# Kernel tuning notes

Hardware: AMD Instinct MI355X
Metric: run time of the kernel (lower is better)

Reference implementation:

```python
import jax, jax.numpy as jnp
import numpy as np

B, C, D, H, W = 1, 128, 8, 32, 32
HEADS = 4
DH = C // HEADS
SCALE = DH ** -0.5


def conv1x1(x, Wt, b):
    # 1x1x1 Conv3d == pointwise channel mix: Wt [out,in], x [B,Cin,D,H,W]
    return jnp.einsum('oc,bcdhw->bodhw', Wt, x) + b[None, :, None, None, None]


def setup_inputs() -> dict:
    key = jax.random.key(0)
    ks = jax.random.split(key, 16)
    p = lambda k, shape: jax.random.normal(k, shape, dtype=jnp.float32) * 0.02
    return {
        'feat1': jax.random.normal(ks[0], (B, C, D, H, W), dtype=jnp.float32),
        'feat2': jax.random.normal(ks[1], (B, C, D, H, W), dtype=jnp.float32),
        'Wq': p(ks[2], (C, C)), 'bq': jnp.zeros((C,), jnp.float32),
        'Wk': p(ks[3], (C, C)), 'bk': jnp.zeros((C,), jnp.float32),
        'Wv': p(ks[4], (C, C)), 'bv': jnp.zeros((C,), jnp.float32),
        'Wo': p(ks[5], (C, C)), 'bo': jnp.zeros((C,), jnp.float32),
        'Wg1': p(ks[6], (C, 2 * C)), 'bg1': jnp.zeros((C,), jnp.float32),
        'Wg2': p(ks[7], (C, C)), 'bg2': jnp.zeros((C,), jnp.float32),
    }


def reference(feat1, feat2, Wq, bq, Wk, bk, Wv, bv, Wo, bo, Wg1, bg1, Wg2, bg2):
    N = D * H * W
    q = conv1x1(feat1, Wq, bq).reshape(B, HEADS, DH, N)
    k = conv1x1(feat2, Wk, bk).reshape(B, HEADS, DH, N)
    v = conv1x1(feat2, Wv, bv).reshape(B, HEADS, DH, N)
    # attn[b,h,n,m] = softmax_m( q[:, :, :, n] . k[:, :, :, m] * scale )
    attn = jax.nn.softmax(jnp.einsum('bhcn,bhcm->bhnm', q, k) * SCALE, axis=-1)
    # out[b,h,c,n] = sum_m attn[b,h,n,m] * v[b,h,c,m]
    out = jnp.einsum('bhnm,bhcm->bhcn', attn, v).reshape(B, C, D, H, W)
    attn_out = conv1x1(out, Wo, bo)
    gated_input = jnp.concatenate([attn_out, feat1], axis=1)  # [B,2C,D,H,W]
    gate = jax.nn.sigmoid(conv1x1(jax.nn.relu(conv1x1(gated_input, Wg1, bg1)), Wg2, bg2))
    return gate * feat1 + (1.0 - gate) * attn_out
```

## Files before the change

### kernel.cpp

```cpp
#include <hip/hip_runtime.h>
#include <hip/hip_bf16.h>


typedef __attribute__((ext_vector_type(4))) float f32x4;
typedef __attribute__((ext_vector_type(4))) unsigned u32x4;
typedef __attribute__((ext_vector_type(8))) short s16x8;
typedef __attribute__((ext_vector_type(4))) short s16x4;

#define MFMA_BF16(A,B,C) __builtin_amdgcn_mfma_f32_16x16x32_bf16((A),(B),(C),0,0,0)

static __device__ __forceinline__ float fexp2(float x){
  float r; asm("v_exp_f32 %0, %1" : "=v"(r) : "v"(x)); return r;
}
static __device__ __forceinline__ float frcp(float x){
  float r; asm("v_rcp_f32 %0, %1" : "=v"(r) : "v"(x)); return r;
}
static __device__ __forceinline__ unsigned cvtpk(float lo, float hi){
  unsigned r; asm("v_cvt_pk_bf16_f32 %0, %1, %2" : "=v"(r) : "v"(lo), "v"(hi)); return r;
}
static __device__ __forceinline__ float bf2f(short s){
  return __bfloat162float(__builtin_bit_cast(__hip_bfloat16, s));
}

__device__ __forceinline__ void gll16(const void* g, void* l){
  __builtin_amdgcn_global_load_lds(
      (const __attribute__((address_space(1))) void*)g,
      (__attribute__((address_space(3))) void*)l, 16, 0, 0);
}

__global__ __launch_bounds__(256) void wprep(
    const float* __restrict__ Wq, const float* __restrict__ Wk,
    const float* __restrict__ Wv, const float* __restrict__ Wo,
    const float* __restrict__ Wg1, const float* __restrict__ Wg2,
    __hip_bfloat16* __restrict__ out)
{
  int i = blockIdx.x*256 + threadIdx.x;
  const float SCQ = 0.17677669529663689f * 1.44269504088896340f;
  float v;
  if      (i < 16384) v = Wq[i]*SCQ;
  else if (i < 32768) v = Wk[i-16384];
  else if (i < 49152) v = Wv[i-32768];
  else if (i < 65536) v = Wo[i-49152];
  else if (i < 98304) v = Wg1[i-65536];
  else                v = Wg2[i-98304];
  out[i] = __float2bfloat16(v);
}

__global__ __launch_bounds__(256) void transpose2(
    const float* __restrict__ f1, const float* __restrict__ f2,
    __hip_bfloat16* __restrict__ F1T, __hip_bfloat16* __restrict__ F2T)
{
  const float* in = blockIdx.y ? f2 : f1;
  __hip_bfloat16* out = blockIdx.y ? F2T : F1T;
  __shared__ __hip_bfloat16 tile[64][128];
  int tid = threadIdx.x;
  int n0 = blockIdx.x*64;
  int cq = tid>>4;
  int nq = (tid&15)*4;
  #pragma unroll
  for (int r=0;r<8;r++){
    int c = r*16 + cq;
    f32x4 val = *(const f32x4*)&in[c*8192 + n0 + nq];
    #pragma unroll
    for (int i=0;i<4;i++){
      int n = nq + i;
      tile[n][c ^ ((n&7)<<4)] = __float2bfloat16(val[i]);
    }
  }
  __syncthreads();
  int row = tid>>2;
  int cb  = (tid&3)*32;
  #pragma unroll
  for (int k=0;k<4;k++){
    int c0 = cb + 8*k;
    s16x8 v = *(const s16x8*)&tile[row][c0 ^ ((row&7)<<4)];
    *(s16x8*)&out[(n0+row)*128 + c0] = v;
  }
}

__global__ __launch_bounds__(256) void qkv(
    const __hip_bfloat16* __restrict__ F1T, const __hip_bfloat16* __restrict__ F2T,
    const __hip_bfloat16* __restrict__ Wall,
    const float* __restrict__ bq, const float* __restrict__ bk,
    const float* __restrict__ bv,
    __hip_bfloat16* __restrict__ QT, __hip_bfloat16* __restrict__ KT,
    __hip_bfloat16* __restrict__ Vp)
{
  const float SCQ = 0.17677669529663689f * 1.44269504088896340f;
  int y = blockIdx.y;
  const __hip_bfloat16* A  = (y==0) ? F1T : F2T;
  const __hip_bfloat16* Bw = Wall + y*16384;
  const float* bias = (y==0) ? bq : (y==1) ? bk : bv;
  float bscale = (y==0) ? SCQ : 1.f;

  int tid = threadIdx.x;
  int w = tid>>6, lane = tid&63, g = lane>>4, ln = lane&15;
  int n0 = blockIdx.x*16, o0 = w*32;
  f32x4 acc0 = {0.f,0.f,0.f,0.f}, acc1 = {0.f,0.f,0.f,0.f};
  #pragma unroll
  for (int ck=0; ck<4; ck++){
    s16x8 af  = *(const s16x8*)&A[(n0+ln)*128 + ck*32 + 8*g];
    s16x8 bf0 = *(const s16x8*)&Bw[(o0+ln)*128 + ck*32 + 8*g];
    s16x8 bf1 = *(const s16x8*)&Bw[(o0+16+ln)*128 + ck*32 + 8*g];
    if (y == 2){
      acc0 = MFMA_BF16(bf0, af, acc0);
      acc1 = MFMA_BF16(bf1, af, acc1);
    } else {
      acc0 = MFMA_BF16(af, bf0, acc0);
      acc1 = MFMA_BF16(af, bf1, acc1);
    }
  }
  if (y == 2){
    #pragma unroll
    for (int to=0; to<2; to++){
      f32x4 a = to ? acc1 : acc0;
      #pragma unroll
      for (int r=0;r<4;r++){
        int o = o0 + 16*to + 4*g + r;
        int n = n0 + ln;
        int m63 = n & 63, blk = n >> 6;
        int Gx = (((m63>>5)<<2) | ((m63>>2)&3)) ^ (o & 7);
        int col = blk*64 + Gx*8 + ((m63>>4)&1)*4 + (m63&3);
        Vp[(size_t)o*8192 + col] = __float2bfloat16(a[r] + bias[o]);
      }
    }
  } else {
    __hip_bfloat16* outb = (y==0) ? QT : KT;
    float b0 = bias[o0+ln]*bscale, b1 = bias[o0+16+ln]*bscale;
    #pragma unroll
    for (int to=0; to<2; to++){
      f32x4 a = to ? acc1 : acc0;
      float bb = to ? b1 : b0;
      int o = o0 + 16*to + ln;
      #pragma unroll
      for (int r=0;r<4;r++){
        int n = n0 + 4*g + r;
        outb[n*128 + o] = __float2bfloat16(a[r] + bb);
      }
    }
  }
}

__global__ __launch_bounds__(256, 2) void attn13(
    const __hip_bfloat16* __restrict__ QT, const __hip_bfloat16* __restrict__ KT,
    const __hip_bfloat16* __restrict__ Vp, __hip_bfloat16* __restrict__ OT)
{
  __shared__ short stage[2][8192];

  const int tid = threadIdx.x;
  const int w = tid>>6, lane = tid&63, g = lane>>4, ln = lane&15;
  const int h = blockIdx.y;
  const int nbase = blockIdx.x*64;

  const __hip_bfloat16* Kh = KT + h*32;
  const __hip_bfloat16* Vh = Vp + (size_t)(h*32)*8192;

  s16x8 qf[4];
  #pragma unroll
  for (int j=0;j<4;j++)
    qf[j] = *(const s16x8*)&QT[(size_t)(nbase+16*j+ln)*128 + h*32 + 8*g];

  const __hip_bfloat16* gp[4];
  int ldoff[4];
  #pragma unroll
  for (int u=0; u<4; u++){
    int row = u*16 + (lane>>2);
    int gk  = (lane&3) ^ ((lane>>3)&3);
    gp[u] = &Kh[(size_t)(w*2048 + row)*128 + 8*gk];
    ldoff[u] = w*2048 + u*512;
  }
  short* sb = &stage[0][0];

  #define ISSUE(OFF) { \
    _Pragma("unroll") \
    for (int u=0;u<4;u++){ gll16(gp[u], sb + (OFF) + ldoff[u]); gp[u] += 64*128; } }

  const int kloff = ln*32 + ((g ^ ((ln>>1)&3))<<3);
  int voff[2];
  voff[0] = 8*((g  ) ^ (ln&7));
  voff[1] = 8*((g+4) ^ (ln&7));

  const short* vb[2][2];
  #pragma unroll
  for (int kk=0;kk<2;kk++)
    #pragma unroll
    for (int ct=0;ct<2;ct++)
      vb[kk][ct] = (const short*)Vh + (size_t)(16*ct+ln)*8192 + w*2048 + voff[kk];

  const u32x4 onesw = {0x3F803F80u,0x3F803F80u,0x3F803F80u,0x3F803F80u};
  const s16x8 onesf = __builtin_bit_cast(s16x8, onesw);

  f32x4 acc[2][4];
  #pragma unroll
  for (int ct=0;ct<2;ct++)
    #pragma unroll
    for (int j=0;j<4;j++) acc[ct][j] = (f32x4){0.f,0.f,0.f,0.f};
  f32x4 accS[4];
  #pragma unroll
  for (int j=0;j<4;j++) accS[j] = (f32x4){0.f,0.f,0.f,0.f};

  #define CONSUME(CUR, T) { \
    const short* Kl = sb + (CUR) + w*2048; \
    s16x8 kf0 = *(const s16x8*)&Kl[         kloff]; \
    s16x8 kf1 = *(const s16x8*)&Kl[ 512  +  kloff]; \
    s16x8 kf2 = *(const s16x8*)&Kl[1024  +  kloff]; \
    s16x8 kf3 = *(const s16x8*)&Kl[1536  +  kloff]; \
    const int mo = (T)*64; \
    s16x8 vf00 = *(const s16x8*)(vb[0][0] + mo); \
    s16x8 vf01 = *(const s16x8*)(vb[0][1] + mo); \
    s16x8 vf10 = *(const s16x8*)(vb[1][0] + mo); \
    s16x8 vf11 = *(const s16x8*)(vb[1][1] + mo); \
    const f32x4 z = {0.f,0.f,0.f,0.f}; \
    __builtin_amdgcn_s_setprio(1); \
    f32x4 s00 = MFMA_BF16(kf0, qf[0], z), s01 = MFMA_BF16(kf0, qf[1], z); \
    f32x4 s02 = MFMA_BF16(kf0, qf[2], z), s03 = MFMA_BF16(kf0, qf[3], z); \
    f32x4 s10 = MFMA_BF16(kf1, qf[0], z), s11 = MFMA_BF16(kf1, qf[1], z); \
    f32x4 s12 = MFMA_BF16(kf1, qf[2], z), s13 = MFMA_BF16(kf1, qf[3], z); \
    __builtin_amdgcn_s_setprio(0); \
    s16x8 pb0[4]; \
    _Pragma("unroll") \
    for (int j=0;j<4;j++){ \
      f32x4 sa = (j==0)?s00:(j==1)?s01:(j==2)?s02:s03; \
      f32x4 sc = (j==0)?s10:(j==1)?s11:(j==2)?s12:s13; \
      float e0=fexp2(sa[0]), e1=fexp2(sa[1]), e2=fexp2(sa[2]), e3=fexp2(sa[3]); \
      float f0=fexp2(sc[0]), f1=fexp2(sc[1]), f2=fexp2(sc[2]), f3=fexp2(sc[3]); \
      u32x4 pw; \
      pw[0]=cvtpk(e0,e1); pw[1]=cvtpk(e2,e3); pw[2]=cvtpk(f0,f1); pw[3]=cvtpk(f2,f3); \
      pb0[j] = __builtin_bit_cast(s16x8, pw); \
    } \
    __builtin_amdgcn_s_setprio(1); \
    f32x4 s20 = MFMA_BF16(kf2, qf[0], z), s21 = MFMA_BF16(kf2, qf[1], z); \
    f32x4 s22 = MFMA_BF16(kf2, qf[2], z), s23 = MFMA_BF16(kf2, qf[3], z); \
    f32x4 s30 = MFMA_BF16(kf3, qf[0], z), s31 = MFMA_BF16(kf3, qf[1], z); \
    f32x4 s32 = MFMA_BF16(kf3, qf[2], z), s33 = MFMA_BF16(kf3, qf[3], z); \
    __builtin_amdgcn_s_setprio(0); \
    s16x8 pb1[4]; \
    _Pragma("unroll") \
    for (int j=0;j<4;j++){ \
      f32x4 sa = (j==0)?s20:(j==1)?s21:(j==2)?s22:s23; \
      f32x4 sc = (j==0)?s30:(j==1)?s31:(j==2)?s32:s33; \
      float e0=fexp2(sa[0]), e1=fexp2(sa[1]), e2=fexp2(sa[2]), e3=fexp2(sa[3]); \
      float f0=fexp2(sc[0]), f1=fexp2(sc[1]), f2=fexp2(sc[2]), f3=fexp2(sc[3]); \
      u32x4 pw; \
      pw[0]=cvtpk(e0,e1); pw[1]=cvtpk(e2,e3); pw[2]=cvtpk(f0,f1); pw[3]=cvtpk(f2,f3); \
      pb1[j] = __builtin_bit_cast(s16x8, pw); \
    } \
    __builtin_amdgcn_s_setprio(1); \
    _Pragma("unroll") \
    for (int j=0;j<4;j++){ \
      acc[0][j] = MFMA_BF16(vf00, pb0[j], acc[0][j]); \
      acc[1][j] = MFMA_BF16(vf01, pb0[j], acc[1][j]); \
      acc[0][j] = MFMA_BF16(vf10, pb1[j], acc[0][j]); \
      acc[1][j] = MFMA_BF16(vf11, pb1[j], acc[1][j]); \
      accS[j]   = MFMA_BF16(onesf, pb0[j], accS[j]); \
      accS[j]   = MFMA_BF16(onesf, pb1[j], accS[j]); \
    } \
    __builtin_amdgcn_s_setprio(0); \
  }

  ISSUE(0);
  int cur = 0;
  for (int t=0; t<31; ++t){
    ISSUE(8192 - cur);
    asm volatile("s_waitcnt vmcnt(4)" ::: "memory");
    CONSUME(cur, t);
    cur = 8192 - cur;
  }
  asm volatile("s_waitcnt vmcnt(0)" ::: "memory");
  CONSUME(cur, 31);
  #undef CONSUME
  #undef ISSUE

  __syncthreads();
  float* scr = (float*)sb;
  if (w != 0){
    int base = ((w-1)*64 + lane)*36;
    #pragma unroll
    for (int ct=0; ct<2; ct++)
      #pragma unroll
      for (int j=0;j<4;j++)
        *(f32x4*)&scr[base + (ct*4+j)*4] = acc[ct][j];
    #pragma unroll
    for (int j=0;j<4;j++) scr[base+32+j] = accS[j][0];
  }
  __syncthreads();
  if (w == 0){
    float inv[4];
    #pragma unroll
    for (int j=0;j<4;j++){
      float ps = accS[j][0];
      #pragma unroll
      for (int q=0; q<3; q++) ps += scr[(q*64+lane)*36 + 32 + j];
      inv[j] = frcp(ps);
    }
    #pragma unroll
    for (int ct=0; ct<2; ct++){
      #pragma unroll
      for (int j=0;j<4;j++){
        f32x4 o = acc[ct][j];
        #pragma unroll
        for (int q=0; q<3; q++)
          o += *(const f32x4*)&scr[(q*64+lane)*36 + (ct*4+j)*4];
        unsigned lo = cvtpk(o[0]*inv[j], o[1]*inv[j]);
        unsigned hi = cvtpk(o[2]*inv[j], o[3]*inv[j]);
        unsigned long long pk = ((unsigned long long)hi<<32) | lo;
        *(unsigned long long*)&OT[(size_t)(nbase+16*j+ln)*128 + h*32 + 16*ct + 4*g] = pk;
      }
    }
  }
}

__global__ __launch_bounds__(256) void tail3(
    const __hip_bfloat16* __restrict__ OT, const __hip_bfloat16* __restrict__ F1T,
    const __hip_bfloat16* __restrict__ WOb, const __hip_bfloat16* __restrict__ WG1b,
    const __hip_bfloat16* __restrict__ WG2b,
    const float* __restrict__ bo, const float* __restrict__ bg1,
    const float* __restrict__ bg2,
    const float* __restrict__ feat1, float* __restrict__ out)
{
  __shared__ __hip_bfloat16 aot[16][128];
  __shared__ __hip_bfloat16 g1[16][128];
  int tid = threadIdx.x;
  int w = tid>>6, lane = tid&63, g = lane>>4, ln = lane&15;
  int n0 = blockIdx.x*16, o0 = w*32;

  {
    f32x4 a0 = {0,0,0,0}, a1 = {0,0,0,0};
    #pragma unroll
    for (int ck=0; ck<4; ck++){
      s16x8 af  = *(const s16x8*)&OT[(n0+ln)*128 + ck*32 + 8*g];
      s16x8 bf0 = *(const s16x8*)&WOb[(o0+ln)*128 + ck*32 + 8*g];
      s16x8 bf1 = *(const s16x8*)&WOb[(o0+16+ln)*128 + ck*32 + 8*g];
      a0 = MFMA_BF16(af, bf0, a0);
      a1 = MFMA_BF16(af, bf1, a1);
    }
    float b0 = bo[o0+ln], b1 = bo[o0+16+ln];
    #pragma unroll
    for (int to=0; to<2; to++){
      f32x4 a = to ? a1 : a0;
      float bb = to ? b1 : b0;
      int o = o0 + 16*to + ln;
      #pragma unroll
      for (int r=0;r<4;r++)
        aot[4*g + r][o] = __float2bfloat16(a[r] + bb);
    }
  }
  __syncthreads();

  {
    f32x4 a0 = {0,0,0,0}, a1 = {0,0,0,0};
    #pragma unroll
    for (int ck=0; ck<8; ck++){
      s16x8 af;
      if (ck < 4) af = *(const s16x8*)&aot[ln][ck*32 + 8*g];
      else        af = *(const s16x8*)&F1T[(n0+ln)*128 + (ck-4)*32 + 8*g];
      s16x8 bf0 = *(const s16x8*)&WG1b[(o0+ln)*256 + ck*32 + 8*g];
      s16x8 bf1 = *(const s16x8*)&WG1b[(o0+16+ln)*256 + ck*32 + 8*g];
      a0 = MFMA_BF16(af, bf0, a0);
      a1 = MFMA_BF16(af, bf1, a1);
    }
    float b0 = bg1[o0+ln], b1 = bg1[o0+16+ln];
    #pragma unroll
    for (int to=0; to<2; to++){
      f32x4 a = to ? a1 : a0;
      float bb = to ? b1 : b0;
      int o = o0 + 16*to + ln;
      #pragma unroll
      for (int r=0;r<4;r++)
        g1[4*g + r][o] = __float2bfloat16(fmaxf(a[r] + bb, 0.f));
    }
  }
  __syncthreads();

  {
    f32x4 a0 = {0,0,0,0}, a1 = {0,0,0,0};
    #pragma unroll
    for (int ck=0; ck<4; ck++){
      s16x8 af  = *(const s16x8*)&g1[ln][ck*32 + 8*g];
      s16x8 bf0 = *(const s16x8*)&WG2b[(o0+ln)*128 + ck*32 + 8*g];
      s16x8 bf1 = *(const s16x8*)&WG2b[(o0+16+ln)*128 + ck*32 + 8*g];
      a0 = MFMA_BF16(af, bf0, a0);
      a1 = MFMA_BF16(af, bf1, a1);
    }
    float b0 = bg2[o0+ln], b1 = bg2[o0+16+ln];
    #pragma unroll
    for (int to=0; to<2; to++){
      f32x4 a = to ? a1 : a0;
      float bb = to ? b1 : b0;
      int o = o0 + 16*to + ln;
      #pragma unroll
      for (int r=0;r<4;r++){
        int nl = 4*g + r;
        int n = n0 + nl;
        float v = a[r] + bb;
        float gt = frcp(1.f + fexp2(-1.44269504f*v));
        float f1v = feat1[(size_t)o*8192 + n];
        float ao = bf2f(__builtin_bit_cast(short, aot[nl][o]));
        out[(size_t)o*8192 + n] = gt*f1v + (1.f - gt)*ao;
      }
    }
  }
}

extern "C" void kernel_launch(void* const* d_in, const int* in_sizes, int n_in,
                              void* d_out, int out_size, void* d_ws, size_t ws_size,
                              hipStream_t stream)
{
  const float* feat1 = (const float*)d_in[0];
  const float* feat2 = (const float*)d_in[1];
  const float* Wq = (const float*)d_in[2];  const float* bq = (const float*)d_in[3];
  const float* Wk = (const float*)d_in[4];  const float* bk = (const float*)d_in[5];
  const float* Wv = (const float*)d_in[6];  const float* bv = (const float*)d_in[7];
  const float* Wo = (const float*)d_in[8];  const float* bo = (const float*)d_in[9];
  const float* Wg1 = (const float*)d_in[10]; const float* bg1 = (const float*)d_in[11];
  const float* Wg2 = (const float*)d_in[12]; const float* bg2 = (const float*)d_in[13];

  __hip_bfloat16* WQb  = (__hip_bfloat16*)d_ws;
  __hip_bfloat16* WKb  = WQb + 16384;
  __hip_bfloat16* WVb  = WQb + 32768;
  __hip_bfloat16* WOb  = WQb + 49152;
  __hip_bfloat16* WG1b = WQb + 65536;
  __hip_bfloat16* WG2b = WQb + 98304;
  __hip_bfloat16* F1T  = WQb + 114688;
  __hip_bfloat16* F2T  = F1T + 1048576;
  __hip_bfloat16* QT   = F1T + 2*1048576;
  __hip_bfloat16* KT   = F1T + 3*1048576;
  __hip_bfloat16* Vbf  = F1T + 4*1048576;
  __hip_bfloat16* OT   = F1T + 5*1048576;

  wprep<<<448,256,0,stream>>>(Wq,Wk,Wv,Wo,Wg1,Wg2,WQb);
  transpose2<<<dim3(128,2),256,0,stream>>>(feat1, feat2, F1T, F2T);
  qkv<<<dim3(512,3),256,0,stream>>>(F1T,F2T,WQb,bq,bk,bv,QT,KT,Vbf);
  attn13<<<dim3(128,4),256,0,stream>>>(QT,KT,Vbf,OT);
  tail3<<<512,256,0,stream>>>(OT,F1T,WOb,WG1b,WG2b,bo,bg1,bg2,feat1,(float*)d_out);
}
```

Before: 85.65 us.

## Merge weight prep with transpose and double per-block token tile in projections

```diff
diff --git a/kernel.cpp b/kernel.cpp
--- a/kernel.cpp
+++ b/kernel.cpp
@@ -28,33 +28,32 @@
       (__attribute__((address_space(3))) void*)l, 16, 0, 0);
 }
 
-__global__ __launch_bounds__(256) void wprep(
+__global__ __launch_bounds__(256) void prep(
+    const float* __restrict__ f1, const float* __restrict__ f2,
+    __hip_bfloat16* __restrict__ F1T, __hip_bfloat16* __restrict__ F2T,
     const float* __restrict__ Wq, const float* __restrict__ Wk,
     const float* __restrict__ Wv, const float* __restrict__ Wo,
     const float* __restrict__ Wg1, const float* __restrict__ Wg2,
-    __hip_bfloat16* __restrict__ out)
+    __hip_bfloat16* __restrict__ wout)
 {
-  int i = blockIdx.x*256 + threadIdx.x;
-  const float SCQ = 0.17677669529663689f * 1.44269504088896340f;
-  float v;
-  if      (i < 16384) v = Wq[i]*SCQ;
-  else if (i < 32768) v = Wk[i-16384];
-  else if (i < 49152) v = Wv[i-32768];
-  else if (i < 65536) v = Wo[i-49152];
-  else if (i < 98304) v = Wg1[i-65536];
-  else                v = Wg2[i-98304];
-  out[i] = __float2bfloat16(v);
-}
-
-__global__ __launch_bounds__(256) void transpose2(
-    const float* __restrict__ f1, const float* __restrict__ f2,
-    __hip_bfloat16* __restrict__ F1T, __hip_bfloat16* __restrict__ F2T)
-{
-  const float* in = blockIdx.y ? f2 : f1;
-  __hip_bfloat16* out = blockIdx.y ? F2T : F1T;
   __shared__ __hip_bfloat16 tile[64][128];
   int tid = threadIdx.x;
-  int n0 = blockIdx.x*64;
+  const float SCQ = 0.17677669529663689f * 1.44269504088896340f;
+  if (blockIdx.x >= 256){
+    int i = (blockIdx.x-256)*256 + tid;
+    float v;
+    if      (i < 16384) v = Wq[i]*SCQ;
+    else if (i < 32768) v = Wk[i-16384];
+    else if (i < 49152) v = Wv[i-32768];
+    else if (i < 65536) v = Wo[i-49152];
+    else if (i < 98304) v = Wg1[i-65536];
+    else                v = Wg2[i-98304];
+    wout[i] = __float2bfloat16(v);
+    return;
+  }
+  const float* in = (blockIdx.x >= 128) ? f2 : f1;
+  __hip_bfloat16* out = (blockIdx.x >= 128) ? F2T : F1T;
+  int n0 = (blockIdx.x & 127)*64;
   int cq = tid>>4;
   int nq = (tid&15)*4;
   #pragma unroll
@@ -95,47 +94,58 @@
 
   int tid = threadIdx.x;
   int w = tid>>6, lane = tid&63, g = lane>>4, ln = lane&15;
-  int n0 = blockIdx.x*16, o0 = w*32;
-  f32x4 acc0 = {0.f,0.f,0.f,0.f}, acc1 = {0.f,0.f,0.f,0.f};
+  int n0 = blockIdx.x*32, o0 = w*32;
+  f32x4 acc[2][2];
+  acc[0][0]=(f32x4){0,0,0,0}; acc[0][1]=(f32x4){0,0,0,0};
+  acc[1][0]=(f32x4){0,0,0,0}; acc[1][1]=(f32x4){0,0,0,0};
   #pragma unroll
   for (int ck=0; ck<4; ck++){
-    s16x8 af  = *(const s16x8*)&A[(n0+ln)*128 + ck*32 + 8*g];
     s16x8 bf0 = *(const s16x8*)&Bw[(o0+ln)*128 + ck*32 + 8*g];
     s16x8 bf1 = *(const s16x8*)&Bw[(o0+16+ln)*128 + ck*32 + 8*g];
-    if (y == 2){
-      acc0 = MFMA_BF16(bf0, af, acc0);
-      acc1 = MFMA_BF16(bf1, af, acc1);
-    } else {
-      acc0 = MFMA_BF16(af, bf0, acc0);
-      acc1 = MFMA_BF16(af, bf1, acc1);
+    #pragma unroll
+    for (int nj=0; nj<2; nj++){
+      s16x8 af = *(const s16x8*)&A[(n0+nj*16+ln)*128 + ck*32 + 8*g];
+      if (y == 2){
+        acc[nj][0] = MFMA_BF16(bf0, af, acc[nj][0]);
+        acc[nj][1] = MFMA_BF16(bf1, af, acc[nj][1]);
+      } else {
+        acc[nj][0] = MFMA_BF16(af, bf0, acc[nj][0]);
+        acc[nj][1] = MFMA_BF16(af, bf1, acc[nj][1]);
+      }
     }
   }
   if (y == 2){
     #pragma unroll
-    for (int to=0; to<2; to++){
-      f32x4 a = to ? acc1 : acc0;
-      #pragma unroll
-      for (int r=0;r<4;r++){
-        int o = o0 + 16*to + 4*g + r;
-        int n = n0 + ln;
-        int m63 = n & 63, blk = n >> 6;
-        int Gx = (((m63>>5)<<2) | ((m63>>2)&3)) ^ (o & 7);
-        int col = blk*64 + Gx*8 + ((m63>>4)&1)*4 + (m63&3);
-        Vp[(size_t)o*8192 + col] = __float2bfloat16(a[r] + bias[o]);
+    for (int nj=0; nj<2; nj++){
+      #pragma unroll
+      for (int to=0; to<2; to++){
+        f32x4 a = acc[nj][to];
+        #pragma unroll
+        for (int r=0;r<4;r++){
+          int o = o0 + 16*to + 4*g + r;
+          int n = n0 + nj*16 + ln;
+          int m63 = n & 63, blk = n >> 6;
+          int Gx = (((m63>>5)<<2) | ((m63>>2)&3)) ^ (o & 7);
+          int col = blk*64 + Gx*8 + ((m63>>4)&1)*4 + (m63&3);
+          Vp[(size_t)o*8192 + col] = __float2bfloat16(a[r] + bias[o]);
+        }
       }
     }
   } else {
     __hip_bfloat16* outb = (y==0) ? QT : KT;
     float b0 = bias[o0+ln]*bscale, b1 = bias[o0+16+ln]*bscale;
     #pragma unroll
-    for (int to=0; to<2; to++){
-      f32x4 a = to ? acc1 : acc0;
-      float bb = to ? b1 : b0;
-      int o = o0 + 16*to + ln;
-      #pragma unroll
-      for (int r=0;r<4;r++){
-        int n = n0 + 4*g + r;
-        outb[n*128 + o] = __float2bfloat16(a[r] + bb);
+    for (int nj=0; nj<2; nj++){
+      #pragma unroll
+      for (int to=0; to<2; to++){
+        f32x4 a = acc[nj][to];
+        float bb = to ? b1 : b0;
+        int o = o0 + 16*to + ln;
+        #pragma unroll
+        for (int r=0;r<4;r++){
+          int n = n0 + nj*16 + 4*g + r;
+          outb[n*128 + o] = __float2bfloat16(a[r] + bb);
+        }
       }
     }
   }
@@ -318,85 +328,109 @@
     const float* __restrict__ bg2,
     const float* __restrict__ feat1, float* __restrict__ out)
 {
-  __shared__ __hip_bfloat16 aot[16][128];
-  __shared__ __hip_bfloat16 g1[16][128];
+  __shared__ __hip_bfloat16 aot[32][128];
+  __shared__ __hip_bfloat16 g1[32][128];
   int tid = threadIdx.x;
   int w = tid>>6, lane = tid&63, g = lane>>4, ln = lane&15;
-  int n0 = blockIdx.x*16, o0 = w*32;
+  int n0 = blockIdx.x*32, o0 = w*32;
 
   {
-    f32x4 a0 = {0,0,0,0}, a1 = {0,0,0,0};
+    f32x4 a[2][2];
+    a[0][0]=(f32x4){0,0,0,0}; a[0][1]=(f32x4){0,0,0,0};
+    a[1][0]=(f32x4){0,0,0,0}; a[1][1]=(f32x4){0,0,0,0};
     #pragma unroll
     for (int ck=0; ck<4; ck++){
-      s16x8 af  = *(const s16x8*)&OT[(n0+ln)*128 + ck*32 + 8*g];
       s16x8 bf0 = *(const s16x8*)&WOb[(o0+ln)*128 + ck*32 + 8*g];
       s16x8 bf1 = *(const s16x8*)&WOb[(o0+16+ln)*128 + ck*32 + 8*g];
-      a0 = MFMA_BF16(af, bf0, a0);
-      a1 = MFMA_BF16(af, bf1, a1);
+      #pragma unroll
+      for (int nj=0; nj<2; nj++){
+        s16x8 af = *(const s16x8*)&OT[(n0+nj*16+ln)*128 + ck*32 + 8*g];
+        a[nj][0] = MFMA_BF16(af, bf0, a[nj][0]);
+        a[nj][1] = MFMA_BF16(af, bf1, a[nj][1]);
+      }
     }
     float b0 = bo[o0+ln], b1 = bo[o0+16+ln];
     #pragma unroll
-    for (int to=0; to<2; to++){
-      f32x4 a = to ? a1 : a0;
-      float bb = to ? b1 : b0;
-      int o = o0 + 16*to + ln;
-      #pragma unroll
-      for (int r=0;r<4;r++)
-        aot[4*g + r][o] = __float2bfloat16(a[r] + bb);
+    for (int nj=0; nj<2; nj++){
+      #pragma unroll
+      for (int to=0; to<2; to++){
+        f32x4 av = a[nj][to];
+        float bb = to ? b1 : b0;
+        int o = o0 + 16*to + ln;
+        #pragma unroll
+        for (int r=0;r<4;r++)
+          aot[nj*16 + 4*g + r][o] = __float2bfloat16(av[r] + bb);
+      }
     }
   }
   __syncthreads();
 
   {
-    f32x4 a0 = {0,0,0,0}, a1 = {0,0,0,0};
+    f32x4 a[2][2];
+    a[0][0]=(f32x4){0,0,0,0}; a[0][1]=(f32x4){0,0,0,0};
+    a[1][0]=(f32x4){0,0,0,0}; a[1][1]=(f32x4){0,0,0,0};
     #pragma unroll
     for (int ck=0; ck<8; ck++){
-      s16x8 af;
-      if (ck < 4) af = *(const s16x8*)&aot[ln][ck*32 + 8*g];
-      else        af = *(const s16x8*)&F1T[(n0+ln)*128 + (ck-4)*32 + 8*g];
       s16x8 bf0 = *(const s16x8*)&WG1b[(o0+ln)*256 + ck*32 + 8*g];
       s16x8 bf1 = *(const s16x8*)&WG1b[(o0+16+ln)*256 + ck*32 + 8*g];
-      a0 = MFMA_BF16(af, bf0, a0);
-      a1 = MFMA_BF16(af, bf1, a1);
+      #pragma unroll
+      for (int nj=0; nj<2; nj++){
+        s16x8 af;
+        if (ck < 4) af = *(const s16x8*)&aot[nj*16+ln][ck*32 + 8*g];
+        else        af = *(const s16x8*)&F1T[(n0+nj*16+ln)*128 + (ck-4)*32 + 8*g];
+        a[nj][0] = MFMA_BF16(af, bf0, a[nj][0]);
+        a[nj][1] = MFMA_BF16(af, bf1, a[nj][1]);
+      }
     }
     float b0 = bg1[o0+ln], b1 = bg1[o0+16+ln];
     #pragma unroll
-    for (int to=0; to<2; to++){
-      f32x4 a = to ? a1 : a0;
-      float bb = to ? b1 : b0;
-      int o = o0 + 16*to + ln;
-      #pragma unroll
-      for (int r=0;r<4;r++)
-        g1[4*g + r][o] = __float2bfloat16(fmaxf(a[r] + bb, 0.f));
+    for (int nj=0; nj<2; nj++){
+      #pragma unroll
+      for (int to=0; to<2; to++){
+        f32x4 av = a[nj][to];
+        float bb = to ? b1 : b0;
+        int o = o0 + 16*to + ln;
+        #pragma unroll
+        for (int r=0;r<4;r++)
+          g1[nj*16 + 4*g + r][o] = __float2bfloat16(fmaxf(av[r] + bb, 0.f));
+      }
     }
   }
   __syncthreads();
 
   {
-    f32x4 a0 = {0,0,0,0}, a1 = {0,0,0,0};
+    f32x4 a[2][2];
+    a[0][0]=(f32x4){0,0,0,0}; a[0][1]=(f32x4){0,0,0,0};
+    a[1][0]=(f32x4){0,0,0,0}; a[1][1]=(f32x4){0,0,0,0};
     #pragma unroll
     for (int ck=0; ck<4; ck++){
-      s16x8 af  = *(const s16x8*)&g1[ln][ck*32 + 8*g];
       s16x8 bf0 = *(const s16x8*)&WG2b[(o0+ln)*128 + ck*32 + 8*g];
       s16x8 bf1 = *(const s16x8*)&WG2b[(o0+16+ln)*128 + ck*32 + 8*g];
-      a0 = MFMA_BF16(af, bf0, a0);
-      a1 = MFMA_BF16(af, bf1, a1);
+      #pragma unroll
+      for (int nj=0; nj<2; nj++){
+        s16x8 af = *(const s16x8*)&g1[nj*16+ln][ck*32 + 8*g];
+        a[nj][0] = MFMA_BF16(af, bf0, a[nj][0]);
+        a[nj][1] = MFMA_BF16(af, bf1, a[nj][1]);
+      }
     }
     float b0 = bg2[o0+ln], b1 = bg2[o0+16+ln];
     #pragma unroll
-    for (int to=0; to<2; to++){
-      f32x4 a = to ? a1 : a0;
-      float bb = to ? b1 : b0;
-      int o = o0 + 16*to + ln;
-      #pragma unroll
-      for (int r=0;r<4;r++){
-        int nl = 4*g + r;
-        int n = n0 + nl;
-        float v = a[r] + bb;
-        float gt = frcp(1.f + fexp2(-1.44269504f*v));
-        float f1v = feat1[(size_t)o*8192 + n];
-        float ao = bf2f(__builtin_bit_cast(short, aot[nl][o]));
-        out[(size_t)o*8192 + n] = gt*f1v + (1.f - gt)*ao;
+    for (int nj=0; nj<2; nj++){
+      #pragma unroll
+      for (int to=0; to<2; to++){
+        f32x4 av = a[nj][to];
+        float bb = to ? b1 : b0;
+        int o = o0 + 16*to + ln;
+        #pragma unroll
+        for (int r=0;r<4;r++){
+          int nl = nj*16 + 4*g + r;
+          int n = n0 + nl;
+          float v = av[r] + bb;
+          float gt = frcp(1.f + fexp2(-1.44269504f*v));
+          float f1v = feat1[(size_t)o*8192 + n];
+          float ao = bf2f(__builtin_bit_cast(short, aot[nl][o]));
+          out[(size_t)o*8192 + n] = gt*f1v + (1.f - gt)*ao;
+        }
       }
     }
   }
@@ -428,9 +462,8 @@
   __hip_bfloat16* Vbf  = F1T + 4*1048576;
   __hip_bfloat16* OT   = F1T + 5*1048576;
 
-  wprep<<<448,256,0,stream>>>(Wq,Wk,Wv,Wo,Wg1,Wg2,WQb);
-  transpose2<<<dim3(128,2),256,0,stream>>>(feat1, feat2, F1T, F2T);
-  qkv<<<dim3(512,3),256,0,stream>>>(F1T,F2T,WQb,bq,bk,bv,QT,KT,Vbf);
+  prep<<<704,256,0,stream>>>(feat1,feat2,F1T,F2T,Wq,Wk,Wv,Wo,Wg1,Wg2,WQb);
+  qkv<<<dim3(256,3),256,0,stream>>>(F1T,F2T,WQb,bq,bk,bv,QT,KT,Vbf);
   attn13<<<dim3(128,4),256,0,stream>>>(QT,KT,Vbf,OT);
-  tail3<<<512,256,0,stream>>>(OT,F1T,WOb,WG1b,WG2b,bo,bg1,bg2,feat1,(float*)d_out);
-}
+  tail3<<<256,256,0,stream>>>(OT,F1T,WOb,WG1b,WG2b,bo,bg1,bg2,feat1,(float*)d_out);
+}
```

Measured after the change: 75.71 us. 1.13x faster.
